# Optimization experiments

Hardware: AMD Instinct MI355X
Metric: run time of the kernel (lower is better)

The kernel has to match this reference:

```python
import jax, jax.numpy as jnp
import numpy as np

TAGSET = 50
T = TAGSET + 2      # tag_size incl START/STOP
START = T - 2       # START_TAG = -2
STOP = T - 1        # STOP_TAG = -1
NEG = -10000.0
B, S = 1024, 512


def _constrain(feats):
    # emissions to START/STOP are forbidden
    return feats.at[..., START].set(NEG).at[..., STOP].set(NEG)


def setup_inputs() -> dict:
    key = jax.random.key(0)
    kf, kl, kt, ktr = jax.random.split(key, 4)
    feats = jax.random.normal(kf, (B, S, T), jnp.float32)
    lengths = jax.random.randint(kl, (B,), S // 4, S + 1)
    mask = jnp.arange(S)[None, :] < lengths[:, None]  # bool prefix mask [B,S]
    tags = jax.random.randint(kt, (B, S), 0, TAGSET)
    # learned param: transitions with START/STOP constraints (as reset_parameters, but random base)
    transitions = 0.1 * jax.random.normal(ktr, (T, T), jnp.float32)
    transitions = transitions.at[:, START].set(NEG).at[STOP, :].set(NEG)
    return {"feats": feats, "mask": mask, "tags": tags, "transitions": transitions}


def reference(feats, mask, tags, transitions):
    del tags  # not used by Viterbi decode (forward)
    feats = _constrain(feats)
    b, s, t = feats.shape
    maskb = mask.astype(bool)
    lengths = jnp.maximum(maskb.sum(axis=1), 1)  # [B]

    alpha0 = transitions[START][None, :] + feats[:, 0]  # [B,T]

    def vstep(alpha, xs):
        f_t, m_t = xs  # [B,T], [B]
        scores = alpha[:, :, None] + transitions[None, :, :] + f_t[:, None, :]  # [B,T_prev,T_cur]
        nxt = scores.max(axis=1)
        bp = scores.argmax(axis=1).astype(jnp.int32)  # [B,T]
        alpha = jnp.where(m_t[:, None], nxt, alpha)
        return alpha, bp

    alpha, history = jax.lax.scan(
        vstep, alpha0, (feats[:, 1:].transpose(1, 0, 2), maskb[:, 1:].T)
    )  # history: [S-1,B,T]

    best_last = jnp.argmax(alpha + transitions[:, STOP][None, :], axis=1).astype(jnp.int32)  # [B]

    # pad so hist_pad[pos] == history[pos-1] for pos>=1
    hist_pad = jnp.concatenate([jnp.zeros((1, b, t), jnp.int32), history], axis=0)  # [S,B,T]

    def tb(ptr, xs):
        pos, bp = xs  # scalar, [B,T]
        ptr = jnp.where(pos == lengths - 1, best_last, ptr)
        tag = jnp.where(pos <= lengths - 1, ptr, 0)  # positions past length stay 0
        nxt = jnp.take_along_axis(bp, ptr[:, None], axis=1)[:, 0]
        ptr = jnp.where((pos >= 1) & (pos <= lengths - 1), nxt, ptr)
        return ptr, tag

    _, decoded = jax.lax.scan(tb, best_last, (jnp.arange(s), hist_pad), reverse=True)  # [S,B]
    return decoded.T  # [B,S] int32 best path
```

## Files before the change

kernel.cpp:

```cpp
#include <hip/hip_runtime.h>

#define TT 52
#define NT 50
#define START_TAG 50
#define STOP_TAG 51
#define BB 1024
#define SS 512
#define BPSTR 64

__device__ __forceinline__ int seq_len(const void* mask, int b, int j) {
    int cnt = 0;
    const unsigned* w = (const unsigned*)mask;
    unsigned w0 = w[0];
    unsigned w1 = w[1];
    if (w0 == 0x01010101u) {
        const unsigned char* m = (const unsigned char*)mask + (size_t)b * SS;
        for (int k = j; k < SS; k += 64) cnt += (m[k] != 0);
    } else if (w0 == 0x3f800000u) {
        const float* m = (const float*)mask + (size_t)b * SS;
        for (int k = j; k < SS; k += 64) cnt += (m[k] != 0.f);
    } else if (w1 == 1u) {
        const int* m = (const int*)mask + (size_t)b * SS;
        for (int k = j; k < SS; k += 64) cnt += (m[k] != 0);
    } else {
        const long long* m = (const long long*)mask + (size_t)b * SS;
        for (int k = j; k < SS; k += 64) cnt += (m[k] != 0);
    }
    for (int off = 32; off; off >>= 1) cnt += __shfl_xor(cnt, off, 64);
    return cnt > 0 ? cnt : 1;
}

__device__ __forceinline__ float4 add4(float4 a, float4 b) {
    return make_float4(a.x + b.x, a.y + b.y, a.z + b.z, a.w + b.w);
}
__device__ __forceinline__ float4 max4(float4 a, float4 b) {
    return make_float4(fmaxf(a.x, b.x), fmaxf(a.y, b.y),
                       fmaxf(a.z, b.z), fmaxf(a.w, b.w));
}

#define DP_STEP(FREG, POSV)                                                       \
    {                                                                             \
        a_sh[j] = alpha;                                                          \
        float4 v0_ = add4(A4[0], tt4[0]);                                         \
        float4 v1_ = add4(A4[1], tt4[1]);                                         \
        float4 v2_ = add4(A4[2], tt4[2]);                                         \
        float4 v3_ = add4(A4[3], tt4[3]);                                         \
        float4 v4_ = add4(A4[4], tt4[4]);                                         \
        float4 v5_ = add4(A4[5], tt4[5]);                                         \
        float4 v6_ = add4(A4[6], tt4[6]);                                         \
        float4 v7_ = add4(A4[7], tt4[7]);                                         \
        float4 v8_ = add4(A4[8], tt4[8]);                                         \
        float4 v9_ = add4(A4[9], tt4[9]);                                         \
        float4 v10_ = add4(A4[10], tt4[10]);                                      \
        float4 v11_ = add4(A4[11], tt4[11]);                                      \
        float4 v12_ = add4(A4[12], tt4[12]);                                      \
        float4 m0_ = max4(v0_, v1_);                                              \
        float4 m1_ = max4(v2_, v3_);                                              \
        float4 m2_ = max4(v4_, v5_);                                              \
        float4 m3_ = max4(v6_, v7_);                                              \
        float4 m4_ = max4(v8_, v9_);                                              \
        float4 m5_ = max4(v10_, v11_);                                            \
        float4 p0_ = max4(m0_, m1_);                                              \
        float4 p1_ = max4(m2_, m3_);                                              \
        float4 p2_ = max4(m4_, m5_);                                              \
        float4 r0_ = max4(p0_, p1_);                                              \
        float4 r1_ = max4(p2_, v12_);                                             \
        float4 t_ = max4(r0_, r1_);                                               \
        float bv_ = fmaxf(fmaxf(t_.x, t_.y), fmaxf(t_.z, t_.w));                  \
        alpha = bv_ + (FREG);                                                     \
        wsb[(size_t)(POSV) * 64] = bv_;                                           \
    }

#define TB_STEP_G(PTR, TPOS, BVC, BVS, FS, OB, WSR, FB, K)                        \
    {                                                                             \
        float bvp_ = BVS[K];                                                      \
        float ap_ = bvp_ + FS[K];                                                 \
        float cand_ = ap_ + trans_lds[jr + PTR];                                  \
        float cm_ = (j < NT) ? cand_ : -3.0e38f;                                  \
        float tgt_ = __builtin_bit_cast(float,                                    \
            __builtin_amdgcn_readlane(__builtin_bit_cast(int, BVC), PTR));        \
        unsigned long long bm_ = __ballot(cm_ == tgt_);                           \
        PTR = __ffsll(bm_) - 1;                                                   \
        --TPOS;                                                                   \
        OB[TPOS] = PTR;                                                           \
        BVC = bvp_;                                                               \
        int rc_ = TPOS - 4; rc_ = rc_ < 0 ? 0 : rc_;                              \
        BVS[K] = WSR[(size_t)rc_ * 64 + j];                                       \
        FS[K] = FB[(size_t)rc_ * TT + jc];                                        \
    }

__global__ __launch_bounds__(64, 1) void crf_viterbi_fast1(
    const float* __restrict__ feats,
    const void*  __restrict__ mask,
    const float* __restrict__ trans,
    float* __restrict__ ws,
    int* __restrict__ out)
{
    __shared__ float trans_lds[64 * 53];
    __shared__ __align__(16) float a_sh[64];

    const int b = blockIdx.x;
    const int j = threadIdx.x;
    const int jc = j < NT ? j : NT - 1;
    const int jr = j * 53;
    const float4* A4 = (const float4*)a_sh;

    for (int k = j; k < 64 * 53; k += 64) {
        int r = k / 53, c = k - r * 53;
        float v = -3.0e38f;
        if (r < NT && c < TT) v = trans[r * TT + c];
        trans_lds[k] = v;
    }

    const int len = seq_len(mask, b, j);

    float4 tt4[13];
#pragma unroll
    for (int r = 0; r < 13; ++r) {
        float c0 = trans[(4 * r + 0) * TT + j];
        float c1 = (4 * r + 1 < NT) ? trans[(4 * r + 1) * TT + j] : -3.0e38f;
        float c2 = (4 * r + 2 < NT) ? trans[(4 * r + 2) * TT + j] : -3.0e38f;
        float c3 = (4 * r + 3 < NT) ? trans[(4 * r + 3) * TT + j] : -3.0e38f;
        tt4[r] = make_float4(c0, c1, c2, c3);
    }

    const float* fp = feats + ((size_t)b * SS) * TT + jc;
    float* wsb = ws + ((size_t)b * SS) * 64 + j;
    const float bvi = trans[START_TAG * TT + jc];
    float alpha = bvi + fp[0];
    wsb[0] = bvi;

#define FLD(P) fp[(size_t)((P) < SS ? (P) : SS - 1) * TT]
    float fA0 = FLD(1), fA1 = FLD(2), fA2 = FLD(3), fA3 = FLD(4);
    float fB0 = FLD(5), fB1 = FLD(6), fB2 = FLD(7), fB3 = FLD(8);

    int pos = 1;
    for (; pos + 7 < len; pos += 8) {
        DP_STEP(fA0, pos + 0)
        DP_STEP(fA1, pos + 1)
        DP_STEP(fA2, pos + 2)
        DP_STEP(fA3, pos + 3)
        fA0 = FLD(pos + 8);  fA1 = FLD(pos + 9);
        fA2 = FLD(pos + 10); fA3 = FLD(pos + 11);
        DP_STEP(fB0, pos + 4)
        DP_STEP(fB1, pos + 5)
        DP_STEP(fB2, pos + 6)
        DP_STEP(fB3, pos + 7)
        fB0 = FLD(pos + 12); fB1 = FLD(pos + 13);
        fB2 = FLD(pos + 14); fB3 = FLD(pos + 15);
    }
    if (pos < len) { DP_STEP(fA0, pos) ++pos; }
    if (pos < len) { DP_STEP(fA1, pos) ++pos; }
    if (pos < len) { DP_STEP(fA2, pos) ++pos; }
    if (pos < len) { DP_STEP(fA3, pos) ++pos; }
    if (pos < len) { DP_STEP(fB0, pos) ++pos; }
    if (pos < len) { DP_STEP(fB1, pos) ++pos; }
    if (pos < len) { DP_STEP(fB2, pos) ++pos; }
#undef FLD

    float v = alpha + trans[jc * TT + STOP_TAG];
    if (j >= NT) v = -3.0e38f;
    int idxb = j < NT ? j : 0;
    for (int off = 32; off; off >>= 1) {
        float vo = __shfl_xor(v, off, 64);
        int   io = __shfl_xor(idxb, off, 64);
        if (vo > v || (vo == v && io < idxb)) { v = vo; idxb = io; }
    }

    __syncthreads();

    int ptr = idxb;
    int* ob = out + (size_t)b * SS;
    ob[len - 1] = ptr;

    const float* wsr = ws + ((size_t)b * SS) * 64;
    const float* fbase = feats + ((size_t)b * SS) * TT;

    float bvs[4], fs[4];
    float bvc = wsr[(size_t)(len - 1) * 64 + j];
#pragma unroll
    for (int k = 0; k < 4; ++k) {
        int r = len - 2 - k; int rc = r < 0 ? 0 : r;
        bvs[k] = wsr[(size_t)rc * 64 + j];
        fs[k]  = fbase[(size_t)rc * TT + jc];
    }

    int tpos = len - 1;
    while (tpos >= 4) {
        TB_STEP_G(ptr, tpos, bvc, bvs, fs, ob, wsr, fbase, 0)
        TB_STEP_G(ptr, tpos, bvc, bvs, fs, ob, wsr, fbase, 1)
        TB_STEP_G(ptr, tpos, bvc, bvs, fs, ob, wsr, fbase, 2)
        TB_STEP_G(ptr, tpos, bvc, bvs, fs, ob, wsr, fbase, 3)
    }
    if (tpos >= 1) TB_STEP_G(ptr, tpos, bvc, bvs, fs, ob, wsr, fbase, 0)
    if (tpos >= 1) TB_STEP_G(ptr, tpos, bvc, bvs, fs, ob, wsr, fbase, 1)
    if (tpos >= 1) TB_STEP_G(ptr, tpos, bvc, bvs, fs, ob, wsr, fbase, 2)

    for (int p = len + j; p < SS; p += 64) ob[p] = 0;
}

__global__ __launch_bounds__(64, 1) void crf_viterbi(
    const float* __restrict__ feats,
    const void*  __restrict__ mask,
    const float* __restrict__ trans,
    int* __restrict__ out)
{
    __shared__ unsigned char bp_sh[SS * BPSTR];

    const int b = blockIdx.x;
    const int j = threadIdx.x;
    const int jc = j < NT ? j : NT - 1;

    const int len = seq_len(mask, b, j);

    float tt[NT];
#pragma unroll
    for (int i = 0; i < NT; ++i) tt[i] = trans[i * TT + j];

    const float* fp = feats + ((size_t)b * SS) * TT + jc;
    float alpha = trans[START_TAG * TT + jc] + fp[0];
    float fnext = fp[TT];

    for (int pos = 1; pos < len; ++pos) {
        const float f = fnext;
        { int np = pos + 1 < SS ? pos + 1 : SS - 1; fnext = fp[(size_t)np * TT]; }

        float best[4] = { -3.0e38f, -3.0e38f, -3.0e38f, -3.0e38f };
        int   bidx[4] = { 0, 0, 0, 0 };
        const int abits = __builtin_bit_cast(int, alpha);
#pragma unroll
        for (int i = 0; i < NT; ++i) {
            int ab = __builtin_amdgcn_readlane(abits, i);
            float s = __builtin_bit_cast(float, ab) + tt[i];
            const int c = i & 3;
            if (s > best[c]) { best[c] = s; bidx[c] = i; }
        }
        float bv = best[0]; int bi = bidx[0];
        if (best[1] > bv || (best[1] == bv && bidx[1] < bi)) { bv = best[1]; bi = bidx[1]; }
        if (best[2] > bv || (best[2] == bv && bidx[2] < bi)) { bv = best[2]; bi = bidx[2]; }
        if (best[3] > bv || (best[3] == bv && bidx[3] < bi)) { bv = best[3]; bi = bidx[3]; }

        alpha = bv + f;
        bp_sh[pos * BPSTR + j] = (unsigned char)bi;
    }

    float v = alpha + trans[jc * TT + STOP_TAG];
    if (j >= NT) v = -3.0e38f;
    int idx = j < NT ? j : 0;
    for (int off = 32; off; off >>= 1) {
        float vo = __shfl_xor(v, off, 64);
        int   io = __shfl_xor(idx, off, 64);
        if (vo > v || (vo == v && io < idx)) { v = vo; idx = io; }
    }

    __syncthreads();

    int ptr = idx;
    int* ob = out + (size_t)b * SS;
    for (int pos = len - 1; pos >= 1; --pos) {
        if (j == 0) ob[pos] = ptr;
        ptr = (int)bp_sh[pos * BPSTR + ptr];
    }
    if (j == 0) ob[0] = ptr;

    for (int p = len + j; p < SS; p += 64) ob[p] = 0;
}

extern "C" void kernel_launch(void* const* d_in, const int* in_sizes, int n_in,
                              void* d_out, int out_size, void* d_ws, size_t ws_size,
                              hipStream_t stream) {
    const float* feats = (const float*)d_in[0];
    const void*  mask  = d_in[1];
    const float* trans = (const float*)d_in[3];
    int* out = (int*)d_out;

    const size_t need = (size_t)BB * SS * 64 * sizeof(float);
    if (ws_size >= need) {
        crf_viterbi_fast1<<<dim3(BB), dim3(64), 0, stream>>>(feats, mask, trans,
                                                             (float*)d_ws, out);
    } else {
        crf_viterbi<<<dim3(BB), dim3(64), 0, stream>>>(feats, mask, trans, out);
    }
}
```

Measured before the change: 180.3 us.

## Replace LDS alpha broadcast with DPP row-rotate and cross-row shuffles

The Viterbi DP step no longer writes alpha to shared memory and reads it back as float4s. Instead, each lane gathers all 64 alpha values through three cross-row shuffles and fifteen DPP row-rotate moves. Each DPP move is fused into an add with a per-lane transition value that was pre-permuted to match the rotated source lane. The aim is to take the LDS store/load round trip off the serial recurrence's critical path. In exchange, each step adds 64 register adds and 3 ds_bpermute-style shuffles, plus 64 transition registers per lane, which raises register pressure.

```diff
diff --git a/kernel.cpp b/kernel.cpp
--- a/kernel.cpp
+++ b/kernel.cpp
@@ -30,45 +30,40 @@
     return cnt > 0 ? cnt : 1;
 }
 
-__device__ __forceinline__ float4 add4(float4 a, float4 b) {
-    return make_float4(a.x + b.x, a.y + b.y, a.z + b.z, a.w + b.w);
-}
-__device__ __forceinline__ float4 max4(float4 a, float4 b) {
-    return make_float4(fmaxf(a.x, b.x), fmaxf(a.y, b.y),
-                       fmaxf(a.z, b.z), fmaxf(a.w, b.w));
-}
+#define RR(R, K, BREG)                                                            \
+    s_[16 * (R) + (K)] = __builtin_bit_cast(float,                                \
+        __builtin_amdgcn_mov_dpp((BREG), 0x120 | (K), 0xF, 0xF, true))            \
+        + tt_[R][K];
+
+#define EXPAND16(R, BREG)                                                         \
+    s_[16 * (R) + 0] = __builtin_bit_cast(float, (BREG)) + tt_[R][0];             \
+    RR(R, 1, BREG)  RR(R, 2, BREG)  RR(R, 3, BREG)  RR(R, 4, BREG)               \
+    RR(R, 5, BREG)  RR(R, 6, BREG)  RR(R, 7, BREG)  RR(R, 8, BREG)               \
+    RR(R, 9, BREG)  RR(R, 10, BREG) RR(R, 11, BREG) RR(R, 12, BREG)              \
+    RR(R, 13, BREG) RR(R, 14, BREG) RR(R, 15, BREG)
 
 #define DP_STEP(FREG, POSV)                                                       \
     {                                                                             \
-        a_sh[j] = alpha;                                                          \
-        float4 v0_ = add4(A4[0], tt4[0]);                                         \
-        float4 v1_ = add4(A4[1], tt4[1]);                                         \
-        float4 v2_ = add4(A4[2], tt4[2]);                                         \
-        float4 v3_ = add4(A4[3], tt4[3]);                                         \
-        float4 v4_ = add4(A4[4], tt4[4]);                                         \
-        float4 v5_ = add4(A4[5], tt4[5]);                                         \
-        float4 v6_ = add4(A4[6], tt4[6]);                                         \
-        float4 v7_ = add4(A4[7], tt4[7]);                                         \
-        float4 v8_ = add4(A4[8], tt4[8]);                                         \
-        float4 v9_ = add4(A4[9], tt4[9]);                                         \
-        float4 v10_ = add4(A4[10], tt4[10]);                                      \
-        float4 v11_ = add4(A4[11], tt4[11]);                                      \
-        float4 v12_ = add4(A4[12], tt4[12]);                                      \
-        float4 m0_ = max4(v0_, v1_);                                              \
-        float4 m1_ = max4(v2_, v3_);                                              \
-        float4 m2_ = max4(v4_, v5_);                                              \
-        float4 m3_ = max4(v6_, v7_);                                              \
-        float4 m4_ = max4(v8_, v9_);                                              \
-        float4 m5_ = max4(v10_, v11_);                                            \
-        float4 p0_ = max4(m0_, m1_);                                              \
-        float4 p1_ = max4(m2_, m3_);                                              \
-        float4 p2_ = max4(m4_, m5_);                                              \
-        float4 r0_ = max4(p0_, p1_);                                              \
-        float4 r1_ = max4(p2_, v12_);                                             \
-        float4 t_ = max4(r0_, r1_);                                               \
-        float bv_ = fmaxf(fmaxf(t_.x, t_.y), fmaxf(t_.z, t_.w));                  \
+        const int ab_ = __builtin_bit_cast(int, alpha);                           \
+        const int b1_ = __shfl_xor(ab_, 16, 64);                                  \
+        const int b2_ = __shfl_xor(ab_, 32, 64);                                  \
+        const int b3_ = __shfl_xor(ab_, 48, 64);                                  \
+        float s_[64];                                                             \
+        EXPAND16(0, ab_) EXPAND16(1, b1_) EXPAND16(2, b2_) EXPAND16(3, b3_)       \
+        float m_[21];                                                             \
+        _Pragma("unroll")                                                         \
+        for (int q_ = 0; q_ < 21; ++q_)                                           \
+            m_[q_] = fmaxf(fmaxf(s_[3 * q_], s_[3 * q_ + 1]), s_[3 * q_ + 2]);    \
+        float n_[7];                                                              \
+        _Pragma("unroll")                                                         \
+        for (int q_ = 0; q_ < 7; ++q_)                                            \
+            n_[q_] = fmaxf(fmaxf(m_[3 * q_], m_[3 * q_ + 1]), m_[3 * q_ + 2]);    \
+        float t0_ = fmaxf(fmaxf(n_[0], n_[1]), n_[2]);                            \
+        float t1_ = fmaxf(fmaxf(n_[3], n_[4]), n_[5]);                            \
+        float t2_ = fmaxf(n_[6], s_[63]);                                         \
+        float bv_ = fmaxf(fmaxf(t0_, t1_), t2_);                                  \
+        wsb[(size_t)(POSV) * 64] = bv_;                                           \
         alpha = bv_ + (FREG);                                                     \
-        wsb[(size_t)(POSV) * 64] = bv_;                                           \
     }
 
 #define TB_STEP_G(PTR, TPOS, BVC, BVS, FS, OB, WSR, FB, K)                        \
@@ -97,13 +92,11 @@
     int* __restrict__ out)
 {
     __shared__ float trans_lds[64 * 53];
-    __shared__ __align__(16) float a_sh[64];
 
     const int b = blockIdx.x;
     const int j = threadIdx.x;
     const int jc = j < NT ? j : NT - 1;
     const int jr = j * 53;
-    const float4* A4 = (const float4*)a_sh;
 
     for (int k = j; k < 64 * 53; k += 64) {
         int r = k / 53, c = k - r * 53;
@@ -114,14 +107,32 @@
 
     const int len = seq_len(mask, b, j);
 
-    float4 tt4[13];
-#pragma unroll
-    for (int r = 0; r < 13; ++r) {
-        float c0 = trans[(4 * r + 0) * TT + j];
-        float c1 = (4 * r + 1 < NT) ? trans[(4 * r + 1) * TT + j] : -3.0e38f;
-        float c2 = (4 * r + 2 < NT) ? trans[(4 * r + 2) * TT + j] : -3.0e38f;
-        float c3 = (4 * r + 3 < NT) ? trans[(4 * r + 3) * TT + j] : -3.0e38f;
-        tt4[r] = make_float4(c0, c1, c2, c3);
+    int pk_[16];
+    pk_[0] = j;
+    pk_[1]  = __builtin_amdgcn_mov_dpp(j, 0x121, 0xF, 0xF, true);
+    pk_[2]  = __builtin_amdgcn_mov_dpp(j, 0x122, 0xF, 0xF, true);
+    pk_[3]  = __builtin_amdgcn_mov_dpp(j, 0x123, 0xF, 0xF, true);
+    pk_[4]  = __builtin_amdgcn_mov_dpp(j, 0x124, 0xF, 0xF, true);
+    pk_[5]  = __builtin_amdgcn_mov_dpp(j, 0x125, 0xF, 0xF, true);
+    pk_[6]  = __builtin_amdgcn_mov_dpp(j, 0x126, 0xF, 0xF, true);
+    pk_[7]  = __builtin_amdgcn_mov_dpp(j, 0x127, 0xF, 0xF, true);
+    pk_[8]  = __builtin_amdgcn_mov_dpp(j, 0x128, 0xF, 0xF, true);
+    pk_[9]  = __builtin_amdgcn_mov_dpp(j, 0x129, 0xF, 0xF, true);
+    pk_[10] = __builtin_amdgcn_mov_dpp(j, 0x12A, 0xF, 0xF, true);
+    pk_[11] = __builtin_amdgcn_mov_dpp(j, 0x12B, 0xF, 0xF, true);
+    pk_[12] = __builtin_amdgcn_mov_dpp(j, 0x12C, 0xF, 0xF, true);
+    pk_[13] = __builtin_amdgcn_mov_dpp(j, 0x12D, 0xF, 0xF, true);
+    pk_[14] = __builtin_amdgcn_mov_dpp(j, 0x12E, 0xF, 0xF, true);
+    pk_[15] = __builtin_amdgcn_mov_dpp(j, 0x12F, 0xF, 0xF, true);
+
+    float tt_[4][16];
+#pragma unroll
+    for (int r = 0; r < 4; ++r) {
+#pragma unroll
+        for (int k = 0; k < 16; ++k) {
+            int i = pk_[k] ^ (r << 4);
+            tt_[r][k] = (i < NT) ? trans[i * TT + j] : -3.0e38f;
+        }
     }
 
     const float* fp = feats + ((size_t)b * SS) * TT + jc;
```

Result: no change. 179.3 us (-0.6%).
